# Kernel optimization log

Hardware: AMD Instinct MI355X
Metric: run time of the kernel (lower is better)

Reference implementation:

```python
import jax, jax.numpy as jnp
import numpy as np


def _rel_pos_index(q_size: int, k_size: int):
    # static (q_size, k_size) index map into the (2*max(q,k)-1, C) table
    q_coords = np.arange(q_size)[:, None] * max(k_size / q_size, 1.0)
    k_coords = np.arange(k_size)[None, :] * max(q_size / k_size, 1.0)
    rel = q_coords - k_coords + (k_size - 1) * max(q_size / k_size, 1.0)
    return jnp.asarray(rel.astype(np.int64))


def setup_inputs() -> dict:
    key = jax.random.key(0)
    k1, k2, k3, k4 = jax.random.split(key, 4)
    B, qh, qw, kh, kw, C = 8, 64, 64, 64, 64, 64
    L = 2 * 64 - 1  # 127, matches max_rel_dist so no interpolation branch
    return {
        "attn": jax.random.normal(k1, (B, qh * qw, kh * kw), dtype=jnp.float32),
        "q": jax.random.normal(k2, (B, qh * qw, C), dtype=jnp.float32),
        "rel_pos_h": jax.random.normal(k3, (L, C), dtype=jnp.float32),
        "rel_pos_w": jax.random.normal(k4, (L, C), dtype=jnp.float32),
        "q_h": qh, "q_w": qw, "k_h": kh, "k_w": kw,
    }


def reference(attn, q, rel_pos_h, rel_pos_w, q_h, q_w, k_h, k_w):
    B, _, C = q.shape
    # gather relative-position embeddings: (q_h, k_h, C) and (q_w, k_w, C)
    Rh = rel_pos_h[_rel_pos_index(q_h, k_h)]
    Rw = rel_pos_w[_rel_pos_index(q_w, k_w)]
    r_q = q.reshape(B, q_h, q_w, C)
    rel_h = jnp.einsum('bhwc,hkc->bhwk', r_q, Rh)  # (B, q_h, q_w, k_h)
    rel_w = jnp.einsum('bhwc,wkc->bhwk', r_q, Rw)  # (B, q_h, q_w, k_w)
    out = (attn.reshape(B, q_h, q_w, k_h, k_w)
           + rel_h[:, :, :, :, None]
           + rel_w[:, :, :, None, :])
    return out.reshape(B, q_h * q_w, k_h * k_w)
```

## Files before the change

kernel.cpp:

```cpp
#include <hip/hip_runtime.h>


__global__ __launch_bounds__(256) void
addrel_kernel(const float* __restrict__ attn,
              const float* __restrict__ q,
              const float* __restrict__ rph,
              const float* __restrict__ rpw,
              float* __restrict__ out)
{
    const int r   = blockIdx.x;
    const int hw  = r & 4095;
    const int h   = hw >> 6;
    const int w   = hw & 63;
    const int tid = threadIdx.x;

    __shared__ __align__(16) float s_q[64];
    __shared__ __align__(16) float s_rh[64];
    __shared__ __align__(16) float s_rw[64];

    if (tid < 64) s_q[tid] = q[(size_t)r * 64 + tid];
    __syncthreads();

    if (tid < 128) {
        const int   k    = tid & 63;
        const bool  isH  = (tid < 64);
        const float* tab = isH ? rph : rpw;
        const int   base = ((isH ? h : w) - k + 63) << 6;
        const float4* row4 = (const float4*)(tab + base);
        const float4* q4   = (const float4*)s_q;
        float acc = 0.f;
        #pragma unroll
        for (int c = 0; c < 16; ++c) {
            float4 a = row4[c];
            float4 b = q4[c];
            acc += a.x * b.x + a.y * b.y + a.z * b.z + a.w * b.w;
        }
        if (isH) s_rh[k] = acc;
        else     s_rw[k] = acc;
    }
    __syncthreads();

    const float4* attn4 = (const float4*)(attn + (size_t)r * 4096);
    float4*       out4  = (float4*)(out + (size_t)r * 4096);
    const float4* rw4   = (const float4*)s_rw;

    #pragma unroll
    for (int i = tid; i < 1024; i += 256) {
        const int   idx = i << 2;
        const float rh  = s_rh[idx >> 6];
        const float4 rw = rw4[(idx & 63) >> 2];
        float4 a = attn4[i];
        a.x += rh + rw.x;
        a.y += rh + rw.y;
        a.z += rh + rw.z;
        a.w += rh + rw.w;
        out4[i] = a;
    }
}

extern "C" void kernel_launch(void* const* d_in, const int* in_sizes, int n_in,
                              void* d_out, int out_size, void* d_ws, size_t ws_size,
                              hipStream_t stream) {
    const float* attn = (const float*)d_in[0];
    const float* q    = (const float*)d_in[1];
    const float* rph  = (const float*)d_in[2];
    const float* rpw  = (const float*)d_in[3];
    float* out = (float*)d_out;

    const int rows = in_sizes[0] / 4096;

    addrel_kernel<<<rows, 256, 0, stream>>>(attn, q, rph, rpw, out);
}
```

Baseline: 958.4 us.

## Split rel-pos dot products into a tiled pre-pass kernel feeding a streaming add

Moves the per-row relative-position dot products into a separate kernel. Each block stages one 64x64 slice of the h or w table in shared memory and reuses it across 64 query rows, writing rel_h and rel_w to workspace. A second kernel then only streams attn, adds the precomputed biases and writes out. This takes the per-row table gathers and syncs out of the bandwidth-bound add, at the cost of an extra launch and a small workspace round trip. The old single-kernel path remains as a fallback when the workspace is too small.

New measurement: 892.9 us. 1.07x faster.

```diff
diff --git a/kernel.cpp b/kernel.cpp
--- a/kernel.cpp
+++ b/kernel.cpp
@@ -1,5 +1,82 @@
 #include <hip/hip_runtime.h>
 
+
+__global__ __launch_bounds__(256) void
+relgemm_kernel(const float* __restrict__ q,
+               const float* __restrict__ rph,
+               const float* __restrict__ rpw,
+               float* __restrict__ relH,
+               float* __restrict__ relW)
+{
+    const int nPairH = gridDim.x >> 1;
+    const int bid    = blockIdx.x;
+    const bool isH   = bid < nPairH;
+    const int pair   = isH ? bid : bid - nPairH;
+    const int b      = pair >> 6;
+    const int x      = pair & 63;
+    const float* __restrict__ tab = isH ? rph : rpw;
+    float* __restrict__ dst       = isH ? relH : relW;
+
+    __shared__ float s_T[64][65];
+
+    for (int e = threadIdx.x; e < 4096; e += 256) {
+        const int i = e >> 6;
+        const int c = e & 63;
+        s_T[c][i] = tab[((x + i) << 6) + c];
+    }
+    __syncthreads();
+
+    const int wave = threadIdx.x >> 6;
+    const int lane = threadIdx.x & 63;
+    const int ti   = 63 - lane;
+
+    #pragma unroll 2
+    for (int yy = 0; yy < 16; ++yy) {
+        const int y = (wave << 4) + yy;
+        const int row = isH ? ((b << 12) + (x << 6) + y)
+                            : ((b << 12) + (y << 6) + x);
+        const float4* __restrict__ q4 = (const float4*)(q + ((size_t)row << 6));
+
+        float a0 = 0.f, a1 = 0.f, a2 = 0.f, a3 = 0.f;
+        #pragma unroll
+        for (int c4 = 0; c4 < 16; ++c4) {
+            const float4 qv = q4[c4];
+            a0 += qv.x * s_T[4 * c4 + 0][ti];
+            a1 += qv.y * s_T[4 * c4 + 1][ti];
+            a2 += qv.z * s_T[4 * c4 + 2][ti];
+            a3 += qv.w * s_T[4 * c4 + 3][ti];
+        }
+        dst[((size_t)row << 6) + lane] = (a0 + a1) + (a2 + a3);
+    }
+}
+
+__global__ __launch_bounds__(256) void
+stream_kernel(const float* __restrict__ attn,
+              const float* __restrict__ relH,
+              const float* __restrict__ relW,
+              float* __restrict__ out)
+{
+    const size_t r   = blockIdx.x;
+    const int    tid = threadIdx.x;
+
+    const float4* __restrict__ attn4 = (const float4*)(attn + (r << 12));
+    float4*       __restrict__ out4  = (float4*)(out + (r << 12));
+    const float*  __restrict__ rh    = relH + (r << 6);
+    const float4* __restrict__ rw4   = (const float4*)(relW + (r << 6));
+
+    #pragma unroll
+    for (int k = 0; k < 4; ++k) {
+        const int i = tid + (k << 8);
+        const float  rhv = rh[i >> 4];
+        const float4 rwv = rw4[i & 15];
+        float4 a = attn4[i];
+        a.x += rhv + rwv.x;
+        a.y += rhv + rwv.y;
+        a.z += rhv + rwv.z;
+        a.w += rhv + rwv.w;
+        out4[i] = a;
+    }
+}
 
 __global__ __launch_bounds__(256) void
 addrel_kernel(const float* __restrict__ attn,
@@ -47,13 +124,13 @@
     #pragma unroll
     for (int i = tid; i < 1024; i += 256) {
         const int   idx = i << 2;
-        const float rh  = s_rh[idx >> 6];
+        const float rhv = s_rh[idx >> 6];
         const float4 rw = rw4[(idx & 63) >> 2];
         float4 a = attn4[i];
-        a.x += rh + rw.x;
-        a.y += rh + rw.y;
-        a.z += rh + rw.z;
-        a.w += rh + rw.w;
+        a.x += rhv + rw.x;
+        a.y += rhv + rw.y;
+        a.z += rhv + rw.z;
+        a.w += rhv + rw.w;
         out4[i] = a;
     }
 }
@@ -67,7 +144,16 @@
     const float* rpw  = (const float*)d_in[3];
     float* out = (float*)d_out;
 
-    const int rows = in_sizes[0] / 4096;
+    const int    rows     = in_sizes[0] / 4096;
+    const size_t relElems = (size_t)rows * 64;
 
-    addrel_kernel<<<rows, 256, 0, stream>>>(attn, q, rph, rpw, out);
+    if (ws_size >= 2 * relElems * sizeof(float)) {
+        float* relH = (float*)d_ws;
+        float* relW = relH + relElems;
+        const int B = rows >> 12;
+        relgemm_kernel<<<2 * B * 64, 256, 0, stream>>>(q, rph, rpw, relH, relW);
+        stream_kernel<<<rows, 256, 0, stream>>>(attn, relH, relW, out);
+    } else {
+        addrel_kernel<<<rows, 256, 0, stream>>>(attn, q, rph, rpw, out);
+    }
 }
```
